# Performance work log

Measured on AMD Instinct MI355X. Metric: run time of the kernel, lower is better.

The kernel has to match this reference:

```python
import jax, jax.numpy as jnp
import numpy as np
from jax import lax

T, R, W, F_CWT, E, H, HG, NC, K = 16, 200, 50, 32, 128, 256, 256, 2, 20


def _make_wavelets():
    t = np.linspace(-1.0, 1.0, W)
    w0 = 6.0
    freqs = np.linspace(1.0, W / 2.0, F_CWT)
    wr = np.zeros((F_CWT, 1, W), np.float32)
    wi = np.zeros((F_CWT, 1, W), np.float32)
    for i, s in enumerate(freqs):
        norm = s ** (-0.5) * np.pi ** (-0.25)
        ts = t / s
        psi = norm * np.exp(1j * w0 * ts) * np.exp(-0.5 * ts ** 2)
        wr[i, 0] = psi.real.astype(np.float32)
        wi[i, 0] = psi.imag.astype(np.float32)
    return jnp.asarray(wr), jnp.asarray(wi)


def setup_inputs() -> dict:
    key = jax.random.key(0)
    ks = jax.random.split(key, 20)
    wr, wi = _make_wavelets()
    s = 0.05
    inp = {
        "time_windows": jax.random.normal(ks[0], (T, R, W), jnp.float32),
        "wav_real": wr, "wav_imag": wi,
        "conv1_w": jax.random.normal(ks[1], (16, 1, 3, 3), jnp.float32) * s,
        "conv1_b": jnp.zeros((16,), jnp.float32),
        "bn1_g": jnp.ones((16,), jnp.float32), "bn1_b": jnp.zeros((16,), jnp.float32),
        "conv2_w": jax.random.normal(ks[2], (32, 16, 3, 3), jnp.float32) * s,
        "conv2_b": jnp.zeros((32,), jnp.float32),
        "bn2_g": jnp.ones((32,), jnp.float32), "bn2_b": jnp.zeros((32,), jnp.float32),
        "fc_w": jax.random.normal(ks[3], (E, 32), jnp.float32) * s,
        "fc_b": jnp.zeros((E,), jnp.float32),
        "q_w": jax.random.normal(ks[4], (E, E), jnp.float32) * s,
        "q_b": jnp.zeros((E,), jnp.float32),
        "k_w": jax.random.normal(ks[5], (E, E), jnp.float32) * s,
        "k_b": jnp.zeros((E,), jnp.float32),
        "gcn1_w": jax.random.normal(ks[6], (E, H), jnp.float32) * s,
        "gcn1_b": jnp.zeros((H,), jnp.float32),
        "gcn2_w": jax.random.normal(ks[7], (H, H), jnp.float32) * s,
        "gcn2_b": jnp.zeros((H,), jnp.float32),
        "gru_wih": jax.random.normal(ks[8], (3 * HG, H), jnp.float32) * s,
        "gru_whh": jax.random.normal(ks[9], (3 * HG, HG), jnp.float32) * s,
        "gru_bih": jnp.zeros((3 * HG,), jnp.float32),
        "gru_bhh": jnp.zeros((3 * HG,), jnp.float32),
        "cls_w": jax.random.normal(ks[10], (NC, HG), jnp.float32) * s,
        "cls_b": jnp.zeros((NC,), jnp.float32),
    }
    return inp


def _conv_bn_relu_pool(x, w, b, g, beta):
    # conv2d k3 pad1, training-mode BN, relu, maxpool2 (floor)
    x = lax.conv_general_dilated(x, w, (1, 1), ((1, 1), (1, 1)),
                                 dimension_numbers=("NCHW", "OIHW", "NCHW"))
    x = x + b[None, :, None, None]
    mu = x.mean((0, 2, 3), keepdims=True)
    var = x.var((0, 2, 3), keepdims=True)
    x = (x - mu) * lax.rsqrt(var + 1e-5) * g[None, :, None, None] + beta[None, :, None, None]
    x = jax.nn.relu(x)
    return lax.reduce_window(x, -jnp.inf, lax.max, (1, 1, 2, 2), (1, 1, 2, 2), "VALID")


def _forward(time_windows, wav_real, wav_imag, conv1_w, conv1_b, bn1_g, bn1_b,
             conv2_w, conv2_b, bn2_g, bn2_b, fc_w, fc_b, q_w, q_b, k_w, k_b,
             gcn1_w, gcn1_b, gcn2_w, gcn2_b, gru_wih, gru_whh, gru_bih, gru_bhh,
             cls_w, cls_b):
    N = T * R
    x = time_windows.reshape(N, 1, W)
    pl = (W - 1) // 2
    pr = (W - 1) - pl  # torch padding='same' (extra on right)
    re = lax.conv_general_dilated(x, wav_real, (1,), [(pl, pr)],
                                  dimension_numbers=("NCH", "OIH", "NCH"))
    im = lax.conv_general_dilated(x, wav_imag, (1,), [(pl, pr)],
                                  dimension_numbers=("NCH", "OIH", "NCH"))
    scal = jnp.sqrt(re * re + im * im)              # [N, F_CWT, W]

    h = scal[:, None]                               # [N,1,F,W]
    h = _conv_bn_relu_pool(h, conv1_w, conv1_b, bn1_g, bn1_b)
    h = _conv_bn_relu_pool(h, conv2_w, conv2_b, bn2_g, bn2_b)
    pooled = h.mean((2, 3))                         # adaptive avg pool -> [N,32]
    emb = pooled @ fc_w.T + fc_b                    # [N,E]
    emb = emb.reshape(T, R, E)

    # sparse-attention graph generation (per window, vectorized over T)
    Q = emb @ q_w.T + q_b
    Kp = emb @ k_w.T + k_b
    attn = jnp.einsum("tre,tse->trs", Q, Kp) / (E ** 0.5)
    attn = jax.nn.leaky_relu(attn, 0.2)
    _, idx = lax.top_k(attn, K)                     # [T,R,K]
    mask = jnp.zeros_like(attn).at[
        jnp.arange(T)[:, None, None], jnp.arange(R)[None, :, None], idx].set(1.0)
    masked = attn * mask
    masked = jnp.where(masked == 0.0, -1e9, masked)
    adj = jax.nn.softmax(masked, axis=-1)           # [T,R,R] row-stochastic, topk-sparse

    # GCNConv x2 with edge weights (PyG gcn_norm: remaining self-loops weight 1,
    ii = jnp.arange(R)
    diag = adj[:, ii, ii]
    adj_sl = adj.at[:, ii, ii].set(jnp.where(diag == 0.0, 1.0, diag))
    Bm = jnp.swapaxes(adj_sl, 1, 2)
    deg = Bm.sum(-1)
    dinv = jnp.where(deg > 0, deg, 1.0) ** -0.5
    An = dinv[:, :, None] * Bm * dinv[:, None, :]   # [T,R,R]
    g = jax.nn.relu(jnp.einsum("trs,tsh->trh", An, emb @ gcn1_w) + gcn1_b)
    g = jax.nn.relu(jnp.einsum("trs,tsh->trh", An, g @ gcn2_w) + gcn2_b)
    g_emb = g.mean(1)                               # [T,H]

    # GRU over the T graph embeddings (batch 1, gate order r,z,n)
    def step(hprev, xt):
        gi = xt @ gru_wih.T + gru_bih
        gh = hprev @ gru_whh.T + gru_bhh
        ir, iz, inn = jnp.split(gi, 3)
        hr, hz, hn = jnp.split(gh, 3)
        r = jax.nn.sigmoid(ir + hr)
        z = jax.nn.sigmoid(iz + hz)
        n = jnp.tanh(inn + r * hn)
        return (1.0 - z) * n + z * hprev, None

    hT, _ = lax.scan(step, jnp.zeros((HG,), emb.dtype), g_emb)
    pred = (hT @ cls_w.T + cls_b)[None]             # [1,NC]

    edge_var = jnp.mean(jnp.var(adj, axis=0, ddof=1))
    avg_adj = adj.mean(0)[None]                     # [1,R,R]
    return pred, avg_adj, edge_var


def reference(time_windows, wav_real, wav_imag, conv1_w, conv1_b, bn1_g, bn1_b,
              conv2_w, conv2_b, bn2_g, bn2_b, fc_w, fc_b, q_w, q_b, k_w, k_b,
              gcn1_w, gcn1_b, gcn2_w, gcn2_b, gru_wih, gru_whh, gru_bih, gru_bhh,
              cls_w, cls_b):
    return _forward(time_windows, wav_real, wav_imag, conv1_w, conv1_b, bn1_g, bn1_b,
                    conv2_w, conv2_b, bn2_g, bn2_b, fc_w, fc_b, q_w, q_b, k_w, k_b,
                    gcn1_w, gcn1_b, gcn2_w, gcn2_b, gru_wih, gru_whh, gru_bih, gru_bhh,
                    cls_w, cls_b)
```

## Files before the change

### kernel.cpp

```cpp
#include <hip/hip_runtime.h>
#include <cfloat>
#include <cmath>

#define T_ 16
#define R_ 200
#define W_ 50
#define FCWT 32
#define E_ 128
#define K_ 20
#define N_ 3200
#define GRU_BLOCKS 6
#define PW 53

__device__ __forceinline__ void waveReduce2(float& a, float& b) {
#pragma unroll
    for (int o = 32; o > 0; o >>= 1) {
        a += __shfl_down(a, o, 64);
        b += __shfl_down(b, o, 64);
    }
}

__global__ __launch_bounds__(256) void transpose_multi_kernel(const float* __restrict__ wih,
                                                              const float* __restrict__ whh,
                                                              const float* __restrict__ qw,
                                                              const float* __restrict__ kw,
                                                              const float* __restrict__ fcw,
                                                              float* __restrict__ wihT,
                                                              float* __restrict__ whhT,
                                                              float* __restrict__ qwT,
                                                              float* __restrict__ kwT,
                                                              float* __restrict__ fcwT,
                                                              int* __restrict__ flags,
                                                              float* __restrict__ out) {
    int b = blockIdx.x, tid = threadIdx.x;
    if (b < 768) {
        int gid = b * 256 + tid; int k = gid / 768, j = gid % 768;
        wihT[gid] = wih[j * 256 + k];
    } else if (b < 1536) {
        int gid = (b - 768) * 256 + tid; int k = gid / 768, j = gid % 768;
        whhT[gid] = whh[j * 256 + k];
    } else if (b < 1600) {
        int gid = (b - 1536) * 256 + tid; int k = gid >> 7, e = gid & 127;
        qwT[gid] = qw[e * 128 + k];
    } else if (b < 1664) {
        int gid = (b - 1600) * 256 + tid; int k = gid >> 7, e = gid & 127;
        kwT[gid] = kw[e * 128 + k];
    } else if (b < 1680) {
        int gid = (b - 1664) * 256 + tid; int c = gid >> 7, e = gid & 127;
        fcwT[gid] = fcw[e * 32 + c];
    } else {
        if (tid < 64) flags[tid] = 0;
        if (tid == 64) out[40002] = 0.f;
    }
}

__global__ __launch_bounds__(256) void cwt_conv1_kernel(const float* __restrict__ x,
                                                        const float* __restrict__ wr,
                                                        const float* __restrict__ wi,
                                                        const float* __restrict__ w1,
                                                        const float* __restrict__ b1,
                                                        float* __restrict__ pooled1max,
                                                        double* __restrict__ psum,
                                                        double* __restrict__ psq) {
    int n = blockIdx.x, tid = threadIdx.x;
    __shared__ float sxp[112];
    __shared__ float swr[FCWT * W_];
    __shared__ float swi[FCWT * W_];
    __shared__ float P1[34 * PW];
    __shared__ float ls[256], lq[256];
    __shared__ float outb[6400];
    if (tid < 112) sxp[tid] = (tid >= 24 && tid < 74) ? x[n * 50 + (tid - 24)] : 0.f;
    for (int idx = tid; idx < FCWT * W_; idx += 256) { swr[idx] = wr[idx]; swi[idx] = wi[idx]; }
    for (int idx = tid; idx < 34 * PW; idx += 256) P1[idx] = 0.f;
    __syncthreads();
    {
        int f = tid >> 3, cg = tid & 7, i0 = cg * 7;
        float xw[7], ar[7], ai[7];
#pragma unroll
        for (int d = 0; d < 7; ++d) { xw[d] = sxp[i0 + d]; ar[d] = 0.f; ai[d] = 0.f; }
        const float* wrf = &swr[f * 50];
        const float* wif = &swi[f * 50];
        for (int j = 0; j < 50; ++j) {
            float wrv = wrf[j], wiv = wif[j];
#pragma unroll
            for (int d = 0; d < 7; ++d) { ar[d] += xw[d] * wrv; ai[d] += xw[d] * wiv; }
#pragma unroll
            for (int d = 0; d < 6; ++d) xw[d] = xw[d + 1];
            xw[6] = sxp[i0 + j + 7];
        }
#pragma unroll
        for (int d = 0; d < 7; ++d) {
            int i = i0 + d;
            if (i < 50) P1[(f + 1) * PW + i + 1] = sqrtf(ar[d] * ar[d] + ai[d] * ai[d]);
        }
    }
    __syncthreads();
    int c = tid & 15, py = tid >> 4;
    float wv[9];
#pragma unroll
    for (int k = 0; k < 9; ++k) wv[k] = w1[c * 9 + k];
    float bias = b1[c];
    const float* r0p = &P1[(2 * py + 0) * PW];
    const float* r1p = &P1[(2 * py + 1) * PW];
    const float* r2p = &P1[(2 * py + 2) * PW];
    const float* r3p = &P1[(2 * py + 3) * PW];
    float c0[4], c1[4];
    c0[0] = r0p[0]; c0[1] = r1p[0]; c0[2] = r2p[0]; c0[3] = r3p[0];
    c1[0] = r0p[1]; c1[1] = r1p[1]; c1[2] = r2p[1]; c1[3] = r3p[1];
    float s = 0.f, q = 0.f, pmax = -FLT_MAX;
    for (int xx = 0; xx < 50; ++xx) {
        float c2[4];
        c2[0] = r0p[xx + 2]; c2[1] = r1p[xx + 2]; c2[2] = r2p[xx + 2]; c2[3] = r3p[xx + 2];
        float v0 = bias + c0[0] * wv[0] + c1[0] * wv[1] + c2[0] * wv[2]
                        + c0[1] * wv[3] + c1[1] * wv[4] + c2[1] * wv[5]
                        + c0[2] * wv[6] + c1[2] * wv[7] + c2[2] * wv[8];
        float v1 = bias + c0[1] * wv[0] + c1[1] * wv[1] + c2[1] * wv[2]
                        + c0[2] * wv[3] + c1[2] * wv[4] + c2[2] * wv[5]
                        + c0[3] * wv[6] + c1[3] * wv[7] + c2[3] * wv[8];
        s += v0 + v1; q += v0 * v0 + v1 * v1;
        float m2 = fmaxf(v0, v1);
        if ((xx & 1) == 0) pmax = m2;
        else outb[(c * 16 + py) * 25 + (xx >> 1)] = fmaxf(pmax, m2);
#pragma unroll
        for (int rr = 0; rr < 4; ++rr) { c0[rr] = c1[rr]; c1[rr] = c2[rr]; }
    }
    ls[tid] = s; lq[tid] = q;
    __syncthreads();
    if (tid < 16) {
        float ss = 0.f, qq = 0.f;
        for (int g = 0; g < 16; ++g) { ss += ls[tid + 16 * g]; qq += lq[tid + 16 * g]; }
        psum[n * 16 + tid] = (double)ss;
        psq[n * 16 + tid] = (double)qq;
    }
    const float4* ob4 = (const float4*)outb;
    float4* p4 = (float4*)(pooled1max + (size_t)n * 6400);
    for (int idx = tid; idx < 1600; idx += 256) p4[idx] = ob4[idx];
}

__global__ __launch_bounds__(256) void bn_finalize_kernel(const double* __restrict__ psum,
                                                          const double* __restrict__ psq,
                                                          const float* __restrict__ g,
                                                          const float* __restrict__ beta,
                                                          float* __restrict__ scale,
                                                          float* __restrict__ shift,
                                                          int C, double inv_count) {
    int c = blockIdx.x, tid = threadIdx.x;
    double s = 0.0, q = 0.0;
    for (int n = tid; n < N_; n += 256) { s += psum[n * C + c]; q += psq[n * C + c]; }
#pragma unroll
    for (int o = 32; o > 0; o >>= 1) { s += __shfl_down(s, o, 64); q += __shfl_down(q, o, 64); }
    __shared__ double sa[4], sb[4];
    int lane = tid & 63, wid = tid >> 6;
    if (lane == 0) { sa[wid] = s; sb[wid] = q; }
    __syncthreads();
    if (tid == 0) {
        s = sa[0] + sa[1] + sa[2] + sa[3];
        q = sb[0] + sb[1] + sb[2] + sb[3];
        double mu = s * inv_count;
        double var = q * inv_count - mu * mu;
        double rstd = 1.0 / sqrt(var + 1e-5);
        double gg = (double)g[c];
        scale[c] = (float)(gg * rstd);
        shift[c] = (float)((double)beta[c] - mu * rstd * gg);
    }
}

__global__ __launch_bounds__(256) void conv2_compute_kernel(const float* __restrict__ pooled1max,
                                                            const float* __restrict__ scale1,
                                                            const float* __restrict__ shift1,
                                                            const float* __restrict__ w2,
                                                            const float* __restrict__ b2,
                                                            float* __restrict__ mm,
                                                            double* __restrict__ psum,
                                                            double* __restrict__ psq) {
    int n = blockIdx.x, tid = threadIdx.x;
    __shared__ float P2[16 * 18 * 28];
    __shared__ float swT[144 * 32];
    __shared__ float ls[256], lq[256];
    for (int idx = tid; idx < 16 * 18 * 28; idx += 256) {
        int ci = idx / 504, rem = idx % 504, yy = rem / 28, xx = rem % 28;
        float v = 0.f;
        if (yy >= 1 && yy <= 16 && xx >= 1 && xx <= 25) {
            float raw = pooled1max[((size_t)n * 16 + ci) * 400 + (yy - 1) * 25 + (xx - 1)];
            v = fmaxf(raw * scale1[ci] + shift1[ci], 0.f);
        }
        P2[idx] = v;
    }
    for (int idx = tid; idx < 4608; idx += 256) {
        int co = idx / 144, r = idx % 144;
        swT[r * 32 + co] = w2[idx];
    }
    __syncthreads();
    int co = tid & 31, pg = tid >> 5;
    float bias = b2[co];
    float acc0[25], acc1[25];
#pragma unroll
    for (int cv = 0; cv < 25; ++cv) { acc0[cv] = bias; acc1[cv] = bias; }
    for (int ci = 0; ci < 16; ++ci) {
        const float* wb = &swT[ci * 288 + co];
        float w[9];
#pragma unroll
        for (int k = 0; k < 9; ++k) w[k] = wb[k * 32];
        const float* base = &P2[ci * 504 + (2 * pg) * 28];
#pragma unroll
        for (int iy = 0; iy < 4; ++iy) {
            float r[28];
            const float4* rp = (const float4*)(base + iy * 28);
#pragma unroll
            for (int m = 0; m < 7; ++m) {
                float4 v4 = rp[m];
                r[4 * m] = v4.x; r[4 * m + 1] = v4.y; r[4 * m + 2] = v4.z; r[4 * m + 3] = v4.w;
            }
            if (iy < 3) {
                int kb = iy * 3;
#pragma unroll
                for (int cv = 0; cv < 25; ++cv)
                    acc0[cv] += r[cv] * w[kb] + r[cv + 1] * w[kb + 1] + r[cv + 2] * w[kb + 2];
            }
            if (iy >= 1) {
                int kb = (iy - 1) * 3;
#pragma unroll
                for (int cv = 0; cv < 25; ++cv)
                    acc1[cv] += r[cv] * w[kb] + r[cv + 1] * w[kb + 1] + r[cv + 2] * w[kb + 2];
            }
        }
    }
    float s = 0.f, q = 0.f;
#pragma unroll
    for (int cv = 0; cv < 25; ++cv) {
        s += acc0[cv] + acc1[cv];
        q += acc0[cv] * acc0[cv] + acc1[cv] * acc1[cv];
    }
#pragma unroll
    for (int pc = 0; pc < 12; ++pc) {
        float v00 = acc0[2 * pc], v01 = acc0[2 * pc + 1];
        float v10 = acc1[2 * pc], v11 = acc1[2 * pc + 1];
        float mx = fmaxf(fmaxf(v00, v01), fmaxf(v10, v11));
        int cell = pg * 12 + pc;
        mm[((size_t)n * 96 + cell) * 32 + co] = mx;
    }
    ls[tid] = s; lq[tid] = q;
    __syncthreads();
    if (tid < 32) {
        float ss = 0.f, qq = 0.f;
        for (int g2 = 0; g2 < 8; ++g2) { ss += ls[tid + 32 * g2]; qq += lq[tid + 32 * g2]; }
        psum[n * 32 + tid] = (double)ss;
        psq[n * 32 + tid] = (double)qq;
    }
}

__global__ __launch_bounds__(256) void pm_fc_qk_kernel(const float* __restrict__ mm,
                                                       const float* __restrict__ scale,
                                                       const float* __restrict__ shift,
                                                       const float* __restrict__ fcwT,
                                                       const float* __restrict__ fc_b,
                                                       const float* __restrict__ qwT,
                                                       const float* __restrict__ q_b,
                                                       const float* __restrict__ kwT,
                                                       const float* __restrict__ k_b,
                                                       float* __restrict__ emb,
                                                       float* __restrict__ Q,
                                                       float* __restrict__ Kp) {
    int n = blockIdx.x, tid = threadIdx.x;
    int co = tid & 31, grp = tid >> 5;
    __shared__ float red[256];
    __shared__ float pm_s[32];
    __shared__ float se[128];
    float sc = scale[co], sh = shift[co];
    float acc = 0.f;
    for (int j = 0; j < 12; ++j) {
        int cell = grp * 12 + j;
        float mx = mm[((size_t)n * 96 + cell) * 32 + co];
        acc += fmaxf(mx * sc + sh, 0.f);
    }
    red[tid] = acc;
    __syncthreads();
    if (tid < 32) {
        float t = 0.f;
        for (int g = 0; g < 8; ++g) t += red[co + 32 * g];
        pm_s[tid] = t * (1.f / 96.f);
    }
    __syncthreads();
    if (tid < 128) {
        float a = fc_b[tid];
        for (int c = 0; c < 32; ++c) a += pm_s[c] * fcwT[c * 128 + tid];
        se[tid] = a;
        emb[(size_t)n * 128 + tid] = a;
    }
    __syncthreads();
    {
        int e = tid & 127, half = tid >> 7;
        const float* w = half ? kwT : qwT;
        float b = half ? k_b[e] : q_b[e];
        float a = b;
        for (int k = 0; k < 128; ++k) a += se[k] * w[k * 128 + e];
        if (half) Kp[(size_t)n * 128 + e] = a;
        else      Q[(size_t)n * 128 + e] = a;
    }
}

__global__ __launch_bounds__(256) void attn_topk_kernel(const float* __restrict__ Q,
                                                        const float* __restrict__ Kp,
                                                        float* __restrict__ adj) {
    int r = blockIdx.x, t = blockIdx.y, tid = threadIdx.x;
    __shared__ float sq[128];
    __shared__ float sc[200];
    if (tid < 128) sq[tid] = Q[(size_t)(t * 200 + r) * 128 + tid];
    __syncthreads();
    if (tid < 200) {
        const float4* kp4 = (const float4*)(Kp + (size_t)(t * 200 + tid) * 128);
        float acc = 0.f;
#pragma unroll 8
        for (int e4 = 0; e4 < 32; ++e4) {
            float4 k4 = kp4[e4];
            acc += sq[e4 * 4 + 0] * k4.x + sq[e4 * 4 + 1] * k4.y +
                   sq[e4 * 4 + 2] * k4.z + sq[e4 * 4 + 3] * k4.w;
        }
        acc = acc / 11.313708498984761f;
        sc[tid] = (acc >= 0.f) ? acc : 0.2f * acc;
    }
    __syncthreads();
    if (tid < 64) {
        int lane = tid;
        float v[4], w[4];
#pragma unroll
        for (int j = 0; j < 4; ++j) {
            int i = lane + 64 * j;
            float x = (i < 200) ? sc[i] : -FLT_MAX;
            v[j] = x; w[j] = x;
        }
        unsigned sel = 0;
        for (int it = 0; it < K_; ++it) {
            float best = -FLT_MAX; int bidx = 0x7fffffff;
#pragma unroll
            for (int j = 0; j < 4; ++j) {
                int i = lane + 64 * j;
                if (w[j] > best || (w[j] == best && i < bidx)) { best = w[j]; bidx = i; }
            }
#pragma unroll
            for (int off = 32; off > 0; off >>= 1) {
                float ob = __shfl_down(best, off, 64);
                int oi = __shfl_down(bidx, off, 64);
                if (ob > best || (ob == best && oi < bidx)) { best = ob; bidx = oi; }
            }
            bidx = __shfl(bidx, 0, 64);
            if ((bidx & 63) == lane) { int j = bidx >> 6; w[j] = -FLT_MAX; sel |= (1u << j); }
        }
        float mv[4]; float m = -FLT_MAX;
#pragma unroll
        for (int j = 0; j < 4; ++j) {
            int i = lane + 64 * j;
            float x = -1e9f;
            if (i < 200 && ((sel >> j) & 1u)) x = (v[j] == 0.f) ? -1e9f : v[j];
            mv[j] = x; m = fmaxf(m, x);
        }
#pragma unroll
        for (int off = 32; off > 0; off >>= 1) m = fmaxf(m, __shfl_xor(m, off, 64));
        float s = 0.f; float e[4];
#pragma unroll
        for (int j = 0; j < 4; ++j) {
            int i = lane + 64 * j;
            e[j] = (i < 200) ? expf(mv[j] - m) : 0.f;
            s += e[j];
        }
#pragma unroll
        for (int off = 32; off > 0; off >>= 1) s += __shfl_xor(s, off, 64);
        float inv = 1.f / s;
        size_t rowo = (size_t)(t * 200 + r) * 200;
#pragma unroll
        for (int j = 0; j < 4; ++j) {
            int i = lane + 64 * j;
            if (i < 200) adj[rowo + i] = e[j] * inv;
        }
    }
}

__global__ __launch_bounds__(256) void an_tile_kernel(const float* __restrict__ adj,
                                                      float* __restrict__ An) {
    int t = blockIdx.y;
    int tr = blockIdx.x >> 2, tc = blockIdx.x & 3;
    int r0 = tr * 50, s0 = tc * 50;
    int tid = threadIdx.x;
    __shared__ float Tt[50 * 51];
    __shared__ float dr[50], ds[50];
    if (tid < 50 || (tid >= 64 && tid < 114)) {
        int col = (tid < 50) ? (r0 + tid) : (s0 + tid - 64);
        float acc = 0.f;
        for (int s = 0; s < 200; ++s) {
            float v = adj[(size_t)(t * 200 + s) * 200 + col];
            if (s == col) v = (v == 0.f) ? 1.f : v;
            acc += v;
        }
        float d = (acc > 0.f) ? acc : 1.f;
        float di = 1.f / sqrtf(d);
        if (tid < 50) dr[tid] = di;
        else ds[tid - 64] = di;
    }
    for (int idx = tid; idx < 2500; idx += 256) {
        int a = idx / 50, b = idx % 50;
        Tt[a * 51 + b] = adj[(size_t)(t * 200 + s0 + a) * 200 + r0 + b];
    }
    __syncthreads();
    for (int idx = tid; idx < 2500; idx += 256) {
        int rl = idx / 50, sl = idx % 50;
        float v = Tt[sl * 51 + rl];
        if (r0 + rl == s0 + sl) v = (v == 0.f) ? 1.f : v;
        An[(size_t)(t * 200 + r0 + rl) * 200 + s0 + sl] = dr[rl] * v * ds[sl];
    }
}

__global__ __launch_bounds__(256) void linear8_kernel(const float* __restrict__ in,
                                                      const float* __restrict__ w,
                                                      float* __restrict__ out, int IN) {
    int n0 = blockIdx.x * 8, h = threadIdx.x;
    __shared__ float sin_[8 * 256];
    for (int idx = h; idx < 8 * IN; idx += 256) sin_[idx] = in[(size_t)n0 * IN + idx];
    __syncthreads();
    float acc[8];
#pragma unroll
    for (int m = 0; m < 8; ++m) acc[m] = 0.f;
    for (int k = 0; k < IN; ++k) {
        float wv = w[k * 256 + h];
#pragma unroll
        for (int m = 0; m < 8; ++m) acc[m] += sin_[m * IN + k] * wv;
    }
#pragma unroll
    for (int m = 0; m < 8; ++m) out[(size_t)(n0 + m) * 256 + h] = acc[m];
}

__global__ __launch_bounds__(256) void gcn_agg16_kernel(const float* __restrict__ An,
                                                        const float* __restrict__ X,
                                                        const float* __restrict__ b,
                                                        float* __restrict__ out) {
    int t = blockIdx.y, r0 = blockIdx.x * 16, h = threadIdx.x;
    __shared__ float sa[16 * 200];
    int rows = (200 - r0 < 16) ? (200 - r0) : 16;
    for (int idx = h; idx < 3200; idx += 256)
        sa[idx] = (idx < rows * 200) ? An[(size_t)(t * 200 + r0) * 200 + idx] : 0.f;
    __syncthreads();
    const float* Xt = X + (size_t)t * 200 * 256;
    float acc[16];
#pragma unroll
    for (int m = 0; m < 16; ++m) acc[m] = 0.f;
    for (int s = 0; s < 200; ++s) {
        float xv = Xt[s * 256 + h];
#pragma unroll
        for (int m = 0; m < 16; ++m) acc[m] += sa[m * 200 + s] * xv;
    }
    float bb = b[h];
    for (int m = 0; m < rows; ++m)
        out[(size_t)(t * 200 + r0 + m) * 256 + h] = fmaxf(acc[m] + bb, 0.f);
}

__global__ __launch_bounds__(256) void gemb_gi_kernel(const float* __restrict__ g2,
                                                      const float* __restrict__ wihT,
                                                      const float* __restrict__ bih,
                                                      float* __restrict__ GI) {
    int t = blockIdx.x, seg = blockIdx.y, tid = threadIdx.x;
    __shared__ float sg[256];
    {
        float acc = 0.f;
        for (int r = 0; r < 200; ++r) acc += g2[(size_t)(t * 200 + r) * 256 + tid];
        sg[tid] = acc * (1.f / 200.f);
    }
    __syncthreads();
    int j = seg * 256 + tid;
    float acc = bih[j];
    for (int k = 0; k < 256; ++k) acc += sg[k] * wihT[k * 768 + j];
    GI[t * 768 + j] = acc;
}

__global__ __launch_bounds__(256) void gru_cls_kernel(const float* __restrict__ GI,
                                                      const float* __restrict__ whhT,
                                                      const float* __restrict__ bhh,
                                                      const float* __restrict__ cls_w,
                                                      const float* __restrict__ cls_b,
                                                      float* __restrict__ GH,
                                                      int* __restrict__ flags,
                                                      float* __restrict__ out) {
    int b = blockIdx.x, tid = threadIdx.x;
    int jl = tid & 127;
    int kc = tid >> 7;
    int j = b * 128 + jl;
    float wreg[128];
#pragma unroll 16
    for (int k = 0; k < 128; ++k)
        wreg[k] = whhT[(size_t)(kc * 128 + k) * 768 + j];
    __shared__ float hcur[256];
    __shared__ float part[256];
    __shared__ float s0[4], s1[4];
    hcur[tid] = 0.f;
    __syncthreads();
    for (int st = 0; st < 16; ++st) {
        float p = 0.f;
        const float* hb = &hcur[kc * 128];
#pragma unroll 16
        for (int k = 0; k < 128; ++k) p += hb[k] * wreg[k];
        part[tid] = p;
        __syncthreads();
        if (tid < 128) {
            GH[st * 768 + b * 128 + tid] = part[tid] + part[tid + 128];
        }
        __threadfence();
        __syncthreads();
        if (tid == 0)
            __hip_atomic_store(&flags[b], st + 1, __ATOMIC_RELEASE, __HIP_MEMORY_SCOPE_AGENT);
        for (int bb = 0; bb < GRU_BLOCKS; ++bb) {
            while (__hip_atomic_load(&flags[bb], __ATOMIC_ACQUIRE, __HIP_MEMORY_SCOPE_AGENT) <= st)
                __builtin_amdgcn_s_sleep(2);
        }
        float ghr = GH[st * 768 + tid]       + bhh[tid];
        float ghz = GH[st * 768 + 256 + tid] + bhh[256 + tid];
        float ghn = GH[st * 768 + 512 + tid] + bhh[512 + tid];
        float gir = GI[st * 768 + tid];
        float giz = GI[st * 768 + 256 + tid];
        float gin = GI[st * 768 + 512 + tid];
        float r = 1.f / (1.f + expf(-(gir + ghr)));
        float z = 1.f / (1.f + expf(-(giz + ghz)));
        float nn = tanhf(gin + r * ghn);
        float hnew = (1.f - z) * nn + z * hcur[tid];
        __syncthreads();
        hcur[tid] = hnew;
        __syncthreads();
    }
    if (b == 0) {
        float v0 = hcur[tid] * cls_w[tid];
        float v1 = hcur[tid] * cls_w[256 + tid];
        waveReduce2(v0, v1);
        int lane = tid & 63, wid = tid >> 6;
        if (lane == 0) { s0[wid] = v0; s1[wid] = v1; }
        __syncthreads();
        if (tid == 0) {
            out[0] = s0[0] + s0[1] + s0[2] + s0[3] + cls_b[0];
            out[1] = s1[0] + s1[1] + s1[2] + s1[3] + cls_b[1];
        }
    }
}

__global__ __launch_bounds__(256) void edge_kernel(const float* __restrict__ adj,
                                                   float* __restrict__ out) {
    int gid = blockIdx.x * 256 + threadIdx.x;
    float var = 0.f;
    if (gid < 40000) {
        float v[16]; float s = 0.f;
#pragma unroll
        for (int t = 0; t < 16; ++t) { v[t] = adj[t * 40000 + gid]; s += v[t]; }
        float mean = s * (1.f / 16.f);
        float q = 0.f;
#pragma unroll
        for (int t = 0; t < 16; ++t) { float d = v[t] - mean; q += d * d; }
        var = q * (1.f / 15.f);
        out[2 + gid] = mean;
    }
    float dummy = 0.f;
    waveReduce2(var, dummy);
    __shared__ float sa[4];
    int lane = threadIdx.x & 63, wid = threadIdx.x >> 6;
    if (lane == 0) sa[wid] = var;
    __syncthreads();
    if (threadIdx.x == 0) {
        float bs = sa[0] + sa[1] + sa[2] + sa[3];
        atomicAdd(&out[40002], bs * (1.f / 40000.f));
    }
}

extern "C" void kernel_launch(void* const* d_in, const int* in_sizes, int n_in,
                              void* d_out, int out_size, void* d_ws, size_t ws_size,
                              hipStream_t stream) {
    const float* tw      = (const float*)d_in[0];
    const float* wav_r   = (const float*)d_in[1];
    const float* wav_i   = (const float*)d_in[2];
    const float* conv1_w = (const float*)d_in[3];
    const float* conv1_b = (const float*)d_in[4];
    const float* bn1_g   = (const float*)d_in[5];
    const float* bn1_b   = (const float*)d_in[6];
    const float* conv2_w = (const float*)d_in[7];
    const float* conv2_b = (const float*)d_in[8];
    const float* bn2_g   = (const float*)d_in[9];
    const float* bn2_b   = (const float*)d_in[10];
    const float* fc_w    = (const float*)d_in[11];
    const float* fc_b    = (const float*)d_in[12];
    const float* q_w     = (const float*)d_in[13];
    const float* q_b     = (const float*)d_in[14];
    const float* k_w     = (const float*)d_in[15];
    const float* k_b     = (const float*)d_in[16];
    const float* gcn1_w  = (const float*)d_in[17];
    const float* gcn1_b  = (const float*)d_in[18];
    const float* gcn2_w  = (const float*)d_in[19];
    const float* gcn2_b  = (const float*)d_in[20];
    const float* gru_wih = (const float*)d_in[21];
    const float* gru_whh = (const float*)d_in[22];
    const float* gru_bih = (const float*)d_in[23];
    const float* gru_bhh = (const float*)d_in[24];
    const float* cls_w   = (const float*)d_in[25];
    const float* cls_b   = (const float*)d_in[26];
    float* out = (float*)d_out;
    (void)in_sizes; (void)n_in; (void)out_size; (void)ws_size;

    const size_t POOLED1_B = (size_t)N_ * 6400 * 4;
    const size_t MM_B      = (size_t)N_ * 96 * 32 * 4;
    const size_t P1S_B     = (size_t)N_ * 16 * 8;
    const size_t P2S_B     = (size_t)N_ * 32 * 8;
    const size_t WT_B      = (size_t)768 * 256 * 4;

    size_t off = 0;
    char* Wb = (char*)d_ws;
    auto take = [&](size_t bytes) -> char* {
        char* p = Wb + off;
        off += (bytes + 255) & ~(size_t)255;
        return p;
    };
    char*  pooled1U = take(POOLED1_B);
    float* mm    = (float*)take(MM_B);
    double* p1sum = (double*)take(P1S_B);
    double* p1sq  = (double*)take(P1S_B);
    double* p2sum = (double*)take(P2S_B);
    double* p2sq  = (double*)take(P2S_B);
    float* scale1 = (float*)take(64 * 4);
    float* shift1 = (float*)take(64 * 4);
    float* scale2 = (float*)take(64 * 4);
    float* shift2 = (float*)take(64 * 4);
    float* wihT   = (float*)take(WT_B);
    float* whhT   = (float*)take(WT_B);
    float* qwT    = (float*)take(128 * 128 * 4);
    float* kwT    = (float*)take(128 * 128 * 4);
    float* fcwT   = (float*)take(32 * 128 * 4);
    float* GH     = (float*)take((size_t)16 * 768 * 4);
    int*   flags  = (int*)take(256);
    float* emb    = (float*)take((size_t)N_ * 128 * 4);
    float* Q      = (float*)take((size_t)N_ * 128 * 4);
    float* Kp     = (float*)take((size_t)N_ * 128 * 4);

    float* pooled1 = (float*)pooled1U;
    size_t moff = 0;
    auto mtake = [&](size_t bytes) -> float* {
        float* p = (float*)(pooled1U + moff);
        moff += (bytes + 255) & ~(size_t)255;
        return p;
    };
    float* adj   = mtake((size_t)T_ * 200 * 200 * 4);
    float* An    = mtake((size_t)T_ * 200 * 200 * 4);
    float* X1    = mtake((size_t)N_ * 256 * 4);
    float* g1    = mtake((size_t)N_ * 256 * 4);
    float* X2    = mtake((size_t)N_ * 256 * 4);
    float* g2    = mtake((size_t)N_ * 256 * 4);
    float* GI    = mtake((size_t)T_ * 768 * 4);

    transpose_multi_kernel<<<1681, 256, 0, stream>>>(gru_wih, gru_whh, q_w, k_w, fc_w,
                                                     wihT, whhT, qwT, kwT, fcwT,
                                                     flags, out);
    cwt_conv1_kernel<<<N_, 256, 0, stream>>>(tw, wav_r, wav_i, conv1_w, conv1_b,
                                             pooled1, p1sum, p1sq);
    bn_finalize_kernel<<<16, 256, 0, stream>>>(p1sum, p1sq, bn1_g, bn1_b, scale1, shift1,
                                               16, 1.0 / 5120000.0);
    conv2_compute_kernel<<<N_, 256, 0, stream>>>(pooled1, scale1, shift1, conv2_w, conv2_b,
                                                 mm, p2sum, p2sq);
    bn_finalize_kernel<<<32, 256, 0, stream>>>(p2sum, p2sq, bn2_g, bn2_b, scale2, shift2,
                                               32, 1.0 / 1280000.0);
    pm_fc_qk_kernel<<<N_, 256, 0, stream>>>(mm, scale2, shift2, fcwT, fc_b,
                                            qwT, q_b, kwT, k_b, emb, Q, Kp);
    attn_topk_kernel<<<dim3(200, 16), 256, 0, stream>>>(Q, Kp, adj);
    an_tile_kernel<<<dim3(16, 16), 256, 0, stream>>>(adj, An);
    linear8_kernel<<<N_ / 8, 256, 0, stream>>>(emb, gcn1_w, X1, 128);
    gcn_agg16_kernel<<<dim3(13, 16), 256, 0, stream>>>(An, X1, gcn1_b, g1);
    linear8_kernel<<<N_ / 8, 256, 0, stream>>>(g1, gcn2_w, X2, 256);
    gcn_agg16_kernel<<<dim3(13, 16), 256, 0, stream>>>(An, X2, gcn2_b, g2);
    gemb_gi_kernel<<<dim3(16, 3), 256, 0, stream>>>(g2, wihT, gru_bih, GI);
    gru_cls_kernel<<<GRU_BLOCKS, 256, 0, stream>>>(GI, whhT, gru_bhh, cls_w, cls_b,
                                                   GH, flags, out);
    edge_kernel<<<(40000 + 255) / 256, 256, 0, stream>>>(adj, out);
}
```

Before: 858.3 us.

## Fuse GCN1 linear into attention kernel and edge stats into An tile kernel

The attention/top-k kernel now handles four query rows per block, reusing each loaded Kp row across them, and extra blocks in the same launch compute the emb x gcn1_w linear. The edge variance/mean kernel is merged as extra blocks into the An normalization kernel. This cuts two launches and the serial tail, and reduces redundant Kp reads. The cost is a 128-float per-thread register buffer for Kp, which may spill or lower occupancy.

```diff
diff --git a/kernel.cpp b/kernel.cpp
--- a/kernel.cpp
+++ b/kernel.cpp
@@ -299,34 +299,69 @@
     }
 }
 
-__global__ __launch_bounds__(256) void attn_topk_kernel(const float* __restrict__ Q,
-                                                        const float* __restrict__ Kp,
-                                                        float* __restrict__ adj) {
-    int r = blockIdx.x, t = blockIdx.y, tid = threadIdx.x;
-    __shared__ float sq[128];
-    __shared__ float sc[200];
-    if (tid < 128) sq[tid] = Q[(size_t)(t * 200 + r) * 128 + tid];
+__global__ __launch_bounds__(256) void attn_topk_lin_kernel(const float* __restrict__ Q,
+                                                            const float* __restrict__ Kp,
+                                                            const float* __restrict__ emb,
+                                                            const float* __restrict__ gcn1_w,
+                                                            float* __restrict__ adj,
+                                                            float* __restrict__ X1) {
+    int bx = blockIdx.x, t = blockIdx.y, tid = threadIdx.x;
+    __shared__ float sq[4 * 128];
+    __shared__ float sc[4 * 200];
+    __shared__ float sin_[8 * 128];
+    if (bx >= 50) {
+        int n0 = ((bx - 50) * 16 + t) * 8;
+        for (int idx = tid; idx < 8 * 128; idx += 256) sin_[idx] = emb[(size_t)n0 * 128 + idx];
+        __syncthreads();
+        float acc[8];
+#pragma unroll
+        for (int m = 0; m < 8; ++m) acc[m] = 0.f;
+        for (int k = 0; k < 128; ++k) {
+            float wv = gcn1_w[k * 256 + tid];
+#pragma unroll
+            for (int m = 0; m < 8; ++m) acc[m] += sin_[m * 128 + k] * wv;
+        }
+#pragma unroll
+        for (int m = 0; m < 8; ++m) X1[(size_t)(n0 + m) * 256 + tid] = acc[m];
+        return;
+    }
+    int r0 = 4 * bx;
+    for (int idx = tid; idx < 512; idx += 256)
+        sq[idx] = Q[(size_t)(t * 200 + r0 + (idx >> 7)) * 128 + (idx & 127)];
     __syncthreads();
     if (tid < 200) {
         const float4* kp4 = (const float4*)(Kp + (size_t)(t * 200 + tid) * 128);
-        float acc = 0.f;
+        float k4buf[128];
+        float a0 = 0.f, a1 = 0.f, a2 = 0.f, a3 = 0.f;
 #pragma unroll 8
         for (int e4 = 0; e4 < 32; ++e4) {
             float4 k4 = kp4[e4];
-            acc += sq[e4 * 4 + 0] * k4.x + sq[e4 * 4 + 1] * k4.y +
-                   sq[e4 * 4 + 2] * k4.z + sq[e4 * 4 + 3] * k4.w;
-        }
-        acc = acc / 11.313708498984761f;
-        sc[tid] = (acc >= 0.f) ? acc : 0.2f * acc;
-    }
-    __syncthreads();
-    if (tid < 64) {
-        int lane = tid;
+            k4buf[4 * e4] = k4.x; k4buf[4 * e4 + 1] = k4.y;
+            k4buf[4 * e4 + 2] = k4.z; k4buf[4 * e4 + 3] = k4.w;
+        }
+        for (int k = 0; k < 128; ++k) {
+            float kv = k4buf[k];
+            a0 += sq[k] * kv;
+            a1 += sq[128 + k] * kv;
+            a2 += sq[256 + k] * kv;
+            a3 += sq[384 + k] * kv;
+        }
+        const float inv_s = 1.f / 11.313708498984761f;
+        a0 *= inv_s; a1 *= inv_s; a2 *= inv_s; a3 *= inv_s;
+        sc[tid]       = (a0 >= 0.f) ? a0 : 0.2f * a0;
+        sc[200 + tid] = (a1 >= 0.f) ? a1 : 0.2f * a1;
+        sc[400 + tid] = (a2 >= 0.f) ? a2 : 0.2f * a2;
+        sc[600 + tid] = (a3 >= 0.f) ? a3 : 0.2f * a3;
+    }
+    __syncthreads();
+    {
+        int wv2 = tid >> 6, lane = tid & 63;
+        const float* a = &sc[wv2 * 200];
         float v[4], w[4];
 #pragma unroll
         for (int j = 0; j < 4; ++j) {
             int i = lane + 64 * j;
-            float x = (i < 200) ? sc[i] : -FLT_MAX;
+            float x = (i < 200) ? a[i] : -FLT_MAX;
             v[j] = x; w[j] = x;
         }
         unsigned sel = 0;
@@ -366,7 +401,7 @@
 #pragma unroll
         for (int off = 32; off > 0; off >>= 1) s += __shfl_xor(s, off, 64);
         float inv = 1.f / s;
-        size_t rowo = (size_t)(t * 200 + r) * 200;
+        size_t rowo = (size_t)(t * 200 + r0 + wv2) * 200;
 #pragma unroll
         for (int j = 0; j < 4; ++j) {
             int i = lane + 64 * j;
@@ -375,12 +410,38 @@
     }
 }
 
-__global__ __launch_bounds__(256) void an_tile_kernel(const float* __restrict__ adj,
-                                                      float* __restrict__ An) {
-    int t = blockIdx.y;
-    int tr = blockIdx.x >> 2, tc = blockIdx.x & 3;
+__global__ __launch_bounds__(256) void an_tile_edge_kernel(const float* __restrict__ adj,
+                                                           float* __restrict__ An,
+                                                           float* __restrict__ out) {
+    int bx = blockIdx.x, t = blockIdx.y, tid = threadIdx.x;
+    if (bx >= 16) {
+        int gid = ((bx - 16) * 16 + t) * 256 + tid;
+        float var = 0.f;
+        if (gid < 40000) {
+            float v[16]; float s = 0.f;
+#pragma unroll
+            for (int tt = 0; tt < 16; ++tt) { v[tt] = adj[(size_t)tt * 40000 + gid]; s += v[tt]; }
+            float mean = s * (1.f / 16.f);
+            float q = 0.f;
+#pragma unroll
+            for (int tt = 0; tt < 16; ++tt) { float d = v[tt] - mean; q += d * d; }
+            var = q * (1.f / 15.f);
+            out[2 + gid] = mean;
+        }
+        float dummy = 0.f;
+        waveReduce2(var, dummy);
+        __shared__ float sa[4];
+        int lane = tid & 63, wid = tid >> 6;
+        if (lane == 0) sa[wid] = var;
+        __syncthreads();
+        if (tid == 0) {
+            float bs = sa[0] + sa[1] + sa[2] + sa[3];
+            atomicAdd(&out[40002], bs * (1.f / 40000.f));
+        }
+        return;
+    }
+    int tr = bx >> 2, tc = bx & 3;
     int r0 = tr * 50, s0 = tc * 50;
-    int tid = threadIdx.x;
     __shared__ float Tt[50 * 51];
     __shared__ float dr[50], ds[50];
     if (tid < 50 || (tid >= 64 && tid < 114)) {
@@ -534,33 +595,6 @@
             out[0] = s0[0] + s0[1] + s0[2] + s0[3] + cls_b[0];
             out[1] = s1[0] + s1[1] + s1[2] + s1[3] + cls_b[1];
         }
-    }
-}
-
-__global__ __launch_bounds__(256) void edge_kernel(const float* __restrict__ adj,
-                                                   float* __restrict__ out) {
-    int gid = blockIdx.x * 256 + threadIdx.x;
-    float var = 0.f;
-    if (gid < 40000) {
-        float v[16]; float s = 0.f;
-#pragma unroll
-        for (int t = 0; t < 16; ++t) { v[t] = adj[t * 40000 + gid]; s += v[t]; }
-        float mean = s * (1.f / 16.f);
-        float q = 0.f;
-#pragma unroll
-        for (int t = 0; t < 16; ++t) { float d = v[t] - mean; q += d * d; }
-        var = q * (1.f / 15.f);
-        out[2 + gid] = mean;
-    }
-    float dummy = 0.f;
-    waveReduce2(var, dummy);
-    __shared__ float sa[4];
-    int lane = threadIdx.x & 63, wid = threadIdx.x >> 6;
-    if (lane == 0) sa[wid] = var;
-    __syncthreads();
-    if (threadIdx.x == 0) {
-        float bs = sa[0] + sa[1] + sa[2] + sa[3];
-        atomicAdd(&out[40002], bs * (1.f / 40000.f));
     }
 }
 
@@ -659,14 +693,12 @@
                                                32, 1.0 / 1280000.0);
     pm_fc_qk_kernel<<<N_, 256, 0, stream>>>(mm, scale2, shift2, fcwT, fc_b,
                                             qwT, q_b, kwT, k_b, emb, Q, Kp);
-    attn_topk_kernel<<<dim3(200, 16), 256, 0, stream>>>(Q, Kp, adj);
-    an_tile_kernel<<<dim3(16, 16), 256, 0, stream>>>(adj, An);
-    linear8_kernel<<<N_ / 8, 256, 0, stream>>>(emb, gcn1_w, X1, 128);
+    attn_topk_lin_kernel<<<dim3(75, 16), 256, 0, stream>>>(Q, Kp, emb, gcn1_w, adj, X1);
+    an_tile_edge_kernel<<<dim3(26, 16), 256, 0, stream>>>(adj, An, out);
     gcn_agg16_kernel<<<dim3(13, 16), 256, 0, stream>>>(An, X1, gcn1_b, g1);
     linear8_kernel<<<N_ / 8, 256, 0, stream>>>(g1, gcn2_w, X2, 256);
     gcn_agg16_kernel<<<dim3(13, 16), 256, 0, stream>>>(An, X2, gcn2_b, g2);
     gemb_gi_kernel<<<dim3(16, 3), 256, 0, stream>>>(g2, wihT, gru_bih, GI);
     gru_cls_kernel<<<GRU_BLOCKS, 256, 0, stream>>>(GI, whhT, gru_bhh, cls_w, cls_b,
                                                    GH, flags, out);
-    edge_kernel<<<(40000 + 255) / 256, 256, 0, stream>>>(adj, out);
-}
+}
```

After: 876.3 us. 2.1% more time.
